# Kernel tuning notes

Measured on AMD Instinct MI355X. Metric: run time of the kernel, lower is better.

The kernel has to match this reference:

```python
import math
import jax, jax.numpy as jnp
import numpy as np

D = 256      # embedding_dim (= internal_dim, downsample_rate 1)
H = 8        # num_heads
HD = D // H  # head_dim = 32
NTC = 16     # num_text_classes
NIMG = 4096  # image tokens (64x64)
N = NIMG + NTC
B = 2
NKE = 64     # num_k_exclude_rope


def _rope(x, freqs):
    # x: (b, h, n, c); freqs: (n, c//2, 2) = (cos, sin) of complex rotary factors
    b, h, n, c = x.shape
    xp = x.reshape(b, h, n, c // 2, 2)
    cos, sin = freqs[..., 0], freqs[..., 1]
    xr, xi = xp[..., 0], xp[..., 1]
    out_r = xr * cos - xi * sin
    out_i = xr * sin + xi * cos
    return jnp.stack([out_r, out_i], axis=-1).reshape(b, h, n, c)


def _sep_heads(x):
    b, n, c = x.shape
    return x.reshape(b, n, H, c // H).transpose(0, 2, 1, 3)  # (b,h,n,hd)


def setup_inputs() -> dict:
    key = jax.random.key(0)
    ks = jax.random.split(key, 14)
    s = 0.02
    # rotary factors: unit-norm cos/sin pairs
    ang_img = jax.random.uniform(ks[3], (NIMG, HD // 2)) * (2.0 * np.pi)
    ang_txt = jax.random.uniform(ks[4], (NTC, HD // 2)) * (2.0 * np.pi)
    return {
        "q": jax.random.normal(ks[0], (B, N, D), dtype=jnp.float32),
        "k": jax.random.normal(ks[1], (B, N, D), dtype=jnp.float32),
        "v": jax.random.normal(ks[2], (B, N, D), dtype=jnp.float32),
        "freqs_cis_img": jnp.stack([jnp.cos(ang_img), jnp.sin(ang_img)], axis=-1),
        "freqs_cis_txt": jnp.stack([jnp.cos(ang_txt), jnp.sin(ang_txt)], axis=-1),
        "Wq": jax.random.normal(ks[5], (D, D), dtype=jnp.float32) * s,
        "bq": jnp.zeros((D,), dtype=jnp.float32),
        "Wk": jax.random.normal(ks[6], (D, D), dtype=jnp.float32) * s,
        "bk": jnp.zeros((D,), dtype=jnp.float32),
        "Wv": jax.random.normal(ks[7], (D, D), dtype=jnp.float32) * s,
        "bv": jnp.zeros((D,), dtype=jnp.float32),
        "Wo": jax.random.normal(ks[8], (D, D), dtype=jnp.float32) * s,
        "bo": jnp.zeros((D,), dtype=jnp.float32),
        "num_k_exclude_rope": NKE,
    }


def reference(q, k, v, freqs_cis_img, freqs_cis_txt,
              Wq, bq, Wk, bk, Wv, bv, Wo, bo, num_k_exclude_rope):
    q = q @ Wq.T + bq
    k = k @ Wk.T + bk
    v = v @ Wv.T + bv
    q = _sep_heads(q)  # (b,h,n,hd)
    k = _sep_heads(k)
    v = _sep_heads(v)

    # split tokens into image / text regions, apply RoPE separately
    q_img, q_txt = q[:, :, :-NTC, :], q[:, :, -NTC:, :]
    k_img, k_txt = k[:, :, :-NTC, :], k[:, :, -NTC:, :]
    q_img = _rope(q_img, freqs_cis_img)
    k_img = _rope(k_img, freqs_cis_img)
    q_txt = _rope(q_txt, freqs_cis_txt)
    k_txt = _rope(k_txt, freqs_cis_txt)
    q = jnp.concatenate([q_img, q_txt], axis=-2)
    k = jnp.concatenate([k_img, k_txt], axis=-2)

    scale = 1.0 / math.sqrt(HD)
    nke = num_k_exclude_rope
    if nke > 0:
        k_td, k_mem = k[:, :, :-nke, :], k[:, :, -nke:, :]
        v_td, v_mem = v[:, :, :-nke, :], v[:, :, -nke:, :]
        attn = jax.nn.softmax(jnp.einsum('bhqd,bhkd->bhqk', q, k_td) * scale, axis=-1)
        out = jnp.einsum('bhqk,bhkd->bhqd', attn, v_td)
        attn_m = jax.nn.softmax(jnp.einsum('bhqd,bhkd->bhqk', q, k_mem) * scale, axis=-1)
        out = out + jnp.einsum('bhqk,bhkd->bhqd', attn_m, v_mem)
    else:
        attn = jax.nn.softmax(jnp.einsum('bhqd,bhkd->bhqk', q, k) * scale, axis=-1)
        out = jnp.einsum('bhqk,bhkd->bhqd', attn, v)

    b, h, n, hd = out.shape
    out = out.transpose(0, 2, 1, 3).reshape(b, n, h * hd)
    return out @ Wo.T + bo
```

## Files before the change

kernel.cpp:

```cpp
#include <hip/hip_runtime.h>
#include <hip/hip_bf16.h>

#define BN    4112
#define NKR   4160
#define BNP   4160
#define BB    2
#define HH    8
#define NIMG_ 4096
#define NMAIN 4048
#define MROWS 8224
#define QSCALE 0.25505402f

typedef __attribute__((ext_vector_type(8))) short short8;
typedef __attribute__((ext_vector_type(4))) float f32x4;

__device__ __forceinline__ unsigned short f2bs(float x) { return __bfloat16_as_ushort(__float2bfloat16(x)); }
__device__ __forceinline__ unsigned pkbf(float a, float b) {
    __hip_bfloat162 h = __float22bfloat162_rn(make_float2(a, b));
    unsigned u; __builtin_memcpy(&u, &h, 4); return u;
}
__device__ __forceinline__ float fexp2(float x) {
#if __has_builtin(__builtin_amdgcn_exp2f)
    return __builtin_amdgcn_exp2f(x);
#else
    return exp2f(x);
#endif
}

__global__ __launch_bounds__(256)
void qkv_mfma(const float* __restrict__ Aq, const float* __restrict__ Ak, const float* __restrict__ Av,
              const float* __restrict__ Wq, const float* __restrict__ Wk, const float* __restrict__ Wv,
              const float* __restrict__ bq, const float* __restrict__ bk, const float* __restrict__ bv,
              short* __restrict__ Qr, short* __restrict__ Kr, short* __restrict__ Vt,
              const float* __restrict__ fimg, const float* __restrict__ ftxt)
{
    __shared__ __align__(16) short Ws[2][64][72];
    __shared__ __align__(16) short Ds[2][64][72];

    const int mode = blockIdx.z;
    const float* A    = (mode == 0) ? Aq : (mode == 1) ? Ak : Av;
    const float* W    = (mode == 0) ? Wq : (mode == 1) ? Wk : Wv;
    const float* bias = (mode == 0) ? bq : (mode == 1) ? bk : bv;

    const int t    = threadIdx.x;
    const int wave = t >> 6, lane = t & 63, q16 = lane & 15, quad = lane >> 4;
    const int f0 = blockIdx.x * 64;
    const int m0 = blockIdx.y * 64;
    const int sr = t >> 2, sc = (t & 3) * 16;
    const int arow = m0 + sr;
    const bool aval = arow < MROWS;
    const float* wp = W + (size_t)(f0 + sr) * 256 + sc;
    const float* ap = A + (size_t)(aval ? arow : 0) * 256 + sc;

    f32x4 acc[4] = {{0,0,0,0},{0,0,0,0},{0,0,0,0},{0,0,0,0}};

    uint4 wr0, wr1, dr0, dr1;
    {
        float4 a0 = *(const float4*)(wp),     a1 = *(const float4*)(wp + 4);
        float4 a2 = *(const float4*)(wp + 8), a3 = *(const float4*)(wp + 12);
        wr0 = uint4{pkbf(a0.x,a0.y), pkbf(a0.z,a0.w), pkbf(a1.x,a1.y), pkbf(a1.z,a1.w)};
        wr1 = uint4{pkbf(a2.x,a2.y), pkbf(a2.z,a2.w), pkbf(a3.x,a3.y), pkbf(a3.z,a3.w)};
        a0 = *(const float4*)(ap);     a1 = *(const float4*)(ap + 4);
        a2 = *(const float4*)(ap + 8); a3 = *(const float4*)(ap + 12);
        dr0 = uint4{pkbf(a0.x,a0.y), pkbf(a0.z,a0.w), pkbf(a1.x,a1.y), pkbf(a1.z,a1.w)};
        dr1 = uint4{pkbf(a2.x,a2.y), pkbf(a2.z,a2.w), pkbf(a3.x,a3.y), pkbf(a3.z,a3.w)};
    }
    *(uint4*)&Ws[0][sr][sc] = wr0; *(uint4*)&Ws[0][sr][sc + 8] = wr1;
    *(uint4*)&Ds[0][sr][sc] = dr0; *(uint4*)&Ds[0][sr][sc + 8] = dr1;
    __syncthreads();

    #pragma unroll
    for (int ki = 0; ki < 4; ++ki) {
        const int buf = ki & 1;
        if (ki < 3) {
            const int k1 = (ki + 1) * 64;
            float4 a0 = *(const float4*)(wp + k1),     a1 = *(const float4*)(wp + k1 + 4);
            float4 a2 = *(const float4*)(wp + k1 + 8), a3 = *(const float4*)(wp + k1 + 12);
            wr0 = uint4{pkbf(a0.x,a0.y), pkbf(a0.z,a0.w), pkbf(a1.x,a1.y), pkbf(a1.z,a1.w)};
            wr1 = uint4{pkbf(a2.x,a2.y), pkbf(a2.z,a2.w), pkbf(a3.x,a3.y), pkbf(a3.z,a3.w)};
            a0 = *(const float4*)(ap + k1);     a1 = *(const float4*)(ap + k1 + 4);
            a2 = *(const float4*)(ap + k1 + 8); a3 = *(const float4*)(ap + k1 + 12);
            dr0 = uint4{pkbf(a0.x,a0.y), pkbf(a0.z,a0.w), pkbf(a1.x,a1.y), pkbf(a1.z,a1.w)};
            dr1 = uint4{pkbf(a2.x,a2.y), pkbf(a2.z,a2.w), pkbf(a3.x,a3.y), pkbf(a3.z,a3.w)};
        }
        #pragma unroll
        for (int ks = 0; ks < 2; ++ks) {
            const short8 af = *(const short8*)&Ws[buf][wave * 16 + q16][ks * 32 + quad * 8];
            #pragma unroll
            for (int ct = 0; ct < 4; ++ct) {
                const short8 bf = *(const short8*)&Ds[buf][ct * 16 + q16][ks * 32 + quad * 8];
                acc[ct] = __builtin_amdgcn_mfma_f32_16x16x32_bf16(af, bf, acc[ct], 0, 0, 0);
            }
        }
        if (ki < 3) {
            *(uint4*)&Ws[buf ^ 1][sr][sc] = wr0; *(uint4*)&Ws[buf ^ 1][sr][sc + 8] = wr1;
            *(uint4*)&Ds[buf ^ 1][sr][sc] = dr0; *(uint4*)&Ds[buf ^ 1][sr][sc + 8] = dr1;
            __syncthreads();
        }
    }

    const int fbase = f0 + wave * 16 + quad * 4;
    const float4 bb = *(const float4*)(bias + fbase);
    float vs[4][4];
    #pragma unroll
    for (int ct = 0; ct < 4; ++ct) {
        int n = m0 + ct * 16 + q16;
        float v0 = acc[ct][0] + bb.x, v1 = acc[ct][1] + bb.y;
        float v2 = acc[ct][2] + bb.z, v3 = acc[ct][3] + bb.w;
        int b  = (n >= BN) ? 1 : 0;
        int nb = n - b * BN;
        if (mode < 2) {
            int j0 = (fbase & 31) >> 1;
            const float* fr = (nb < NIMG_) ? (fimg + ((size_t)nb * 16 + j0) * 2)
                                           : (ftxt + ((size_t)(nb - NIMG_) * 16 + j0) * 2);
            float4 cs = *(const float4*)fr;
            float r0 = v0 * cs.x - v1 * cs.y, i0 = v0 * cs.y + v1 * cs.x;
            float r1 = v2 * cs.z - v3 * cs.w, i1 = v2 * cs.w + v3 * cs.z;
            v0 = r0; v1 = i0; v2 = r1; v3 = i1;
        }
        if (mode == 2) {
            vs[ct][0] = v0; vs[ct][1] = v1; vs[ct][2] = v2; vs[ct][3] = v3;
            continue;
        }
        if (n >= MROWS) continue;
        const int h = (fbase >> 5) & 7, hd = fbase & 31;
        if (mode == 0) {
            unsigned short* op = (unsigned short*)Qr + (((size_t)(b * HH + h) * BN + nb) * 32 + hd);
            *(uint2*)op = uint2{pkbf(v0 * QSCALE, v1 * QSCALE), pkbf(v2 * QSCALE, v3 * QSCALE)};
        } else {
            int nk = nb + ((nb >= NMAIN) ? 48 : 0);
            unsigned short* op = (unsigned short*)Kr + (((size_t)(b * HH + h) * NKR + nk) * 32 + hd);
            *(uint2*)op = uint2{pkbf(v0, v1), pkbf(v2, v3)};
        }
    }

    if (mode == 2) {
        short (*Tr)[72] = Ds[0];
        const int fl = wave * 16 + quad * 4;
        #pragma unroll
        for (int ct = 0; ct < 4; ++ct) {
            const int nl = ct * 16 + q16;
            Tr[fl + 0][nl] = (short)f2bs(vs[ct][0]);
            Tr[fl + 1][nl] = (short)f2bs(vs[ct][1]);
            Tr[fl + 2][nl] = (short)f2bs(vs[ct][2]);
            Tr[fl + 3][nl] = (short)f2bs(vs[ct][3]);
        }
        __syncthreads();
        const int h0 = (f0 >> 5) & 7;
        #pragma unroll
        for (int ii = 0; ii < 2; ++ii) {
            const int r  = ii * 32 + (t >> 3);
            const int c8 = (t & 7) * 8;
            const int ng = m0 + c8;
            if (ng < MROWS) {
                uint4 val = *(const uint4*)&Tr[r][c8];
                int b  = (ng >= BN) ? 1 : 0;
                int nb = ng - b * BN;
                int nk = nb + ((nb >= NMAIN) ? 48 : 0);
                int h  = h0 + (r >> 5), hd = r & 31;
                unsigned short* op = (unsigned short*)Vt + ((size_t)(b * HH + h) * 32 + hd) * BNP + nk;
                *(uint4*)op = val;
            }
        }
    }

    if (blockIdx.x == 0 && blockIdx.y < 16 && t < 192) {
        const int bh = blockIdx.y;
        if (mode == 1) {
            short* base = Kr + (size_t)bh * NKR * 32 + (size_t)NMAIN * 32;
            *(uint4*)(base + t * 8) = uint4{0u, 0u, 0u, 0u};
        } else if (mode == 2) {
            short* base = Vt + (size_t)bh * 32 * BNP + (size_t)(t / 6) * BNP + NMAIN + (t % 6) * 8;
            *(uint4*)base = uint4{0u, 0u, 0u, 0u};
        }
    }
}

__global__ __launch_bounds__(256)
void attn_mfma(const short* __restrict__ Qr, const short* __restrict__ Kr,
               const short* __restrict__ Vt, unsigned short* __restrict__ AO)
{
    __shared__ __align__(16) short Ks[3][64][40];
    __shared__ __align__(16) short Vs[3][32][72];
    __shared__ __align__(16) short Ps[2][4][16][72];

    const int t    = threadIdx.x;
    const int wave = t >> 6, lane = t & 63, q16 = lane & 15, quad = lane >> 4;
    const int bh = blockIdx.y;
    const int q  = blockIdx.x * 64 + wave * 16 + q16;
    const int qc = (q < BN) ? q : (BN - 1);
    const short8 qf = *(const short8*)(Qr + ((size_t)bh * BN + qc) * 32 + quad * 8);

    f32x4 oA0 = {0,0,0,0}, oA1 = {0,0,0,0}, oB0 = {0,0,0,0}, oB1 = {0,0,0,0};
    float LA = 0.f, LB = 0.f;

    const int kr = t >> 2, kc = t & 3;
    const int vr = t >> 3, vc = t & 7;
    const short* kg = Kr + (size_t)bh * NKR * 32 + (size_t)kr * 32 + kc * 8;
    const short* vg = Vt + (size_t)bh * 32 * BNP + (size_t)vr * BNP + vc * 8;

    auto qk = [&](int buf, int pb) -> float {
        float lsum = 0.f;
        #pragma unroll
        for (int mt = 0; mt < 4; ++mt) {
            const short8 kf = *(const short8*)&Ks[buf][mt * 16 + q16][quad * 8];
            f32x4 z = {0,0,0,0};
            f32x4 s = __builtin_amdgcn_mfma_f32_16x16x32_bf16(kf, qf, z, 0, 0, 0);
            float p0 = fexp2(s[0]), p1 = fexp2(s[1]), p2 = fexp2(s[2]), p3 = fexp2(s[3]);
            lsum += (p0 + p1) + (p2 + p3);
            *(uint2*)&Ps[pb][wave][q16][mt * 16 + quad * 4] = uint2{pkbf(p0, p1), pkbf(p2, p3)};
        }
        return lsum;
    };
    auto pv = [&](int buf, int pb, f32x4& o0, f32x4& o1) {
        const short8 p0  = *(const short8*)&Ps[pb][wave][q16][quad * 8];
        const short8 p1  = *(const short8*)&Ps[pb][wave][q16][32 + quad * 8];
        const short8 v00 = *(const short8*)&Vs[buf][q16][quad * 8];
        const short8 v01 = *(const short8*)&Vs[buf][q16][32 + quad * 8];
        const short8 v10 = *(const short8*)&Vs[buf][16 + q16][quad * 8];
        const short8 v11 = *(const short8*)&Vs[buf][16 + q16][32 + quad * 8];
        o0 = __builtin_amdgcn_mfma_f32_16x16x32_bf16(v00, p0, o0, 0, 0, 0);
        o0 = __builtin_amdgcn_mfma_f32_16x16x32_bf16(v01, p1, o0, 0, 0, 0);
        o1 = __builtin_amdgcn_mfma_f32_16x16x32_bf16(v10, p0, o1, 0, 0, 0);
        o1 = __builtin_amdgcn_mfma_f32_16x16x32_bf16(v11, p1, o1, 0, 0, 0);
    };

    uint4 kA = *(const uint4*)(kg),        vA = *(const uint4*)(vg);
    *(uint4*)&Ks[0][kr][kc * 8] = kA;  *(uint4*)&Vs[0][vr][vc * 8] = vA;
    __syncthreads();
    kA = *(const uint4*)(kg + 2048);   vA = *(const uint4*)(vg + 64);
    LA += qk(0, 0);
    *(uint4*)&Ks[1][kr][kc * 8] = kA;  *(uint4*)&Vs[1][vr][vc * 8] = vA;
    __syncthreads();
    kA = *(const uint4*)(kg + 2 * 2048); vA = *(const uint4*)(vg + 2 * 64);

    int bc = 0, bn = 1, bp = 2, pc = 0;
    for (int it = 0; it < 64; ++it) {
        uint4 kN, vN;
        const bool pre = (it + 3) <= 64;
        if (pre) { kN = *(const uint4*)(kg + (size_t)(it + 3) * 2048);
                   vN = *(const uint4*)(vg + (it + 3) * 64); }
        float ls = qk(bn, pc ^ 1);
        if (it < 63) LA += ls; else LB += ls;
        pv(bc, pc, oA0, oA1);
        if (it + 2 <= 64) { *(uint4*)&Ks[bp][kr][kc * 8] = kA;
                            *(uint4*)&Vs[bp][vr][vc * 8] = vA; }
        if (pre) { kA = kN; vA = vN; }
        __syncthreads();
        int tmp = bc; bc = bn; bn = bp; bp = tmp; pc ^= 1;
    }
    pv(bc, pc, oB0, oB1);

    LA += __shfl_xor(LA, 16); LA += __shfl_xor(LA, 32);
    LB += __shfl_xor(LB, 16); LB += __shfl_xor(LB, 32);
    LA -= 48.f;

    if (q < BN) {
        const float iA = 1.f / LA, iB = 1.f / LB;
        const int b = bh >> 3, h = bh & 7;
        unsigned short* ap = AO + ((size_t)b * BN + q) * 256 + h * 32;
        float w0[4], w1[4];
        #pragma unroll
        for (int r = 0; r < 4; ++r) {
            w0[r] = oA0[r] * iA + oB0[r] * iB;
            w1[r] = oA1[r] * iA + oB1[r] * iB;
        }
        *(uint2*)(ap + quad * 4)      = uint2{pkbf(w0[0], w0[1]), pkbf(w0[2], w0[3])};
        *(uint2*)(ap + 16 + quad * 4) = uint2{pkbf(w1[0], w1[1]), pkbf(w1[2], w1[3])};
    }
}

__global__ __launch_bounds__(256)
void gemm_out(const unsigned short* __restrict__ A, const float* __restrict__ W,
              const float* __restrict__ bias, float* __restrict__ out)
{
    __shared__ __align__(16) short Ws[2][64][72];
    __shared__ __align__(16) short Ds[2][64][72];
    const int t    = threadIdx.x;
    const int wave = t >> 6, lane = t & 63, q16 = lane & 15, quad = lane >> 4;
    const int f0 = blockIdx.x * 64, m0 = blockIdx.y * 64;
    const int sr = t >> 2, sc = (t & 3) * 16;
    const int arow = m0 + sr;
    const bool aval = arow < MROWS;
    const float* wp = W + (size_t)(f0 + sr) * 256 + sc;
    const unsigned short* ap = A + (size_t)(aval ? arow : 0) * 256 + sc;

    f32x4 acc[4] = {{0,0,0,0},{0,0,0,0},{0,0,0,0},{0,0,0,0}};

    uint4 wr0, wr1, dr0, dr1;
    {
        float4 a0 = *(const float4*)(wp),     a1 = *(const float4*)(wp + 4);
        float4 a2 = *(const float4*)(wp + 8), a3 = *(const float4*)(wp + 12);
        wr0 = uint4{pkbf(a0.x,a0.y), pkbf(a0.z,a0.w), pkbf(a1.x,a1.y), pkbf(a1.z,a1.w)};
        wr1 = uint4{pkbf(a2.x,a2.y), pkbf(a2.z,a2.w), pkbf(a3.x,a3.y), pkbf(a3.z,a3.w)};
        dr0 = *(const uint4*)(ap); dr1 = *(const uint4*)(ap + 8);
    }
    *(uint4*)&Ws[0][sr][sc] = wr0; *(uint4*)&Ws[0][sr][sc + 8] = wr1;
    *(uint4*)&Ds[0][sr][sc] = dr0; *(uint4*)&Ds[0][sr][sc + 8] = dr1;
    __syncthreads();

    #pragma unroll
    for (int ki = 0; ki < 4; ++ki) {
        const int buf = ki & 1;
        if (ki < 3) {
            const int k1 = (ki + 1) * 64;
            float4 a0 = *(const float4*)(wp + k1),     a1 = *(const float4*)(wp + k1 + 4);
            float4 a2 = *(const float4*)(wp + k1 + 8), a3 = *(const float4*)(wp + k1 + 12);
            wr0 = uint4{pkbf(a0.x,a0.y), pkbf(a0.z,a0.w), pkbf(a1.x,a1.y), pkbf(a1.z,a1.w)};
            wr1 = uint4{pkbf(a2.x,a2.y), pkbf(a2.z,a2.w), pkbf(a3.x,a3.y), pkbf(a3.z,a3.w)};
            dr0 = *(const uint4*)(ap + k1); dr1 = *(const uint4*)(ap + k1 + 8);
        }
        #pragma unroll
        for (int ks = 0; ks < 2; ++ks) {
            const short8 af = *(const short8*)&Ws[buf][wave * 16 + q16][ks * 32 + quad * 8];
            #pragma unroll
            for (int ct = 0; ct < 4; ++ct) {
                const short8 bf = *(const short8*)&Ds[buf][ct * 16 + q16][ks * 32 + quad * 8];
                acc[ct] = __builtin_amdgcn_mfma_f32_16x16x32_bf16(af, bf, acc[ct], 0, 0, 0);
            }
        }
        if (ki < 3) {
            *(uint4*)&Ws[buf ^ 1][sr][sc] = wr0; *(uint4*)&Ws[buf ^ 1][sr][sc + 8] = wr1;
            *(uint4*)&Ds[buf ^ 1][sr][sc] = dr0; *(uint4*)&Ds[buf ^ 1][sr][sc + 8] = dr1;
            __syncthreads();
        }
    }

    const int fbase = f0 + wave * 16 + quad * 4;
    const float4 bb = *(const float4*)(bias + fbase);
    #pragma unroll
    for (int ct = 0; ct < 4; ++ct) {
        int n = m0 + ct * 16 + q16;
        if (n >= MROWS) continue;
        float* op = out + (size_t)n * 256 + fbase;
        *(float4*)op = float4{acc[ct][0] + bb.x, acc[ct][1] + bb.y,
                              acc[ct][2] + bb.z, acc[ct][3] + bb.w};
    }
}

extern "C" void kernel_launch(void* const* d_in, const int* in_sizes, int n_in,
                              void* d_out, int out_size, void* d_ws, size_t ws_size,
                              hipStream_t stream)
{
    (void)in_sizes; (void)n_in; (void)out_size; (void)ws_size;
    const float* q    = (const float*)d_in[0];
    const float* k    = (const float*)d_in[1];
    const float* v    = (const float*)d_in[2];
    const float* fimg = (const float*)d_in[3];
    const float* ftxt = (const float*)d_in[4];
    const float* Wq   = (const float*)d_in[5];
    const float* bq   = (const float*)d_in[6];
    const float* Wk   = (const float*)d_in[7];
    const float* bk   = (const float*)d_in[8];
    const float* Wv   = (const float*)d_in[9];
    const float* bv   = (const float*)d_in[10];
    const float* Wo   = (const float*)d_in[11];
    const float* bo   = (const float*)d_in[12];

    char* w = (char*)d_ws;
    short*          Qr = (short*)(w);
    short*          Kr = (short*)(w + 4210688);
    short*          Vt = (short*)(w + 8470528);
    unsigned short* AO = (unsigned short*)(w + 12730368);

    qkv_mfma<<<dim3(4, 129, 3), 256, 0, stream>>>(q, k, v, Wq, Wk, Wv, bq, bk, bv,
                                                  Qr, Kr, Vt, fimg, ftxt);
    attn_mfma<<<dim3(65, 16), 256, 0, stream>>>(Qr, Kr, Vt, AO);
    gemm_out<<<dim3(4, 129), 256, 0, stream>>>(AO, Wo, bo, (float*)d_out);
}
```

Measured before the change: 234.4 us.

## Keep softmax probabilities in registers and double-buffer K/V tiles

The attention loop no longer stages P through shared memory. Each pair of QK MFMA outputs is exponentiated, packed to bf16 and fed directly as the B operand of the PV MFMA, with the V fragments gathered to match that register layout. The three-stage K/V ring plus P double buffer becomes a simple two-stage ring, which cuts LDS traffic and footprint. The cost is less software pipelining overlap between QK and PV, plus more scattered 32-bit LDS reads for V.

```diff
diff --git a/kernel.cpp b/kernel.cpp
--- a/kernel.cpp
+++ b/kernel.cpp
@@ -180,9 +180,8 @@
 void attn_mfma(const short* __restrict__ Qr, const short* __restrict__ Kr,
                const short* __restrict__ Vt, unsigned short* __restrict__ AO)
 {
-    __shared__ __align__(16) short Ks[3][64][40];
-    __shared__ __align__(16) short Vs[3][32][72];
-    __shared__ __align__(16) short Ps[2][4][16][72];
+    __shared__ __align__(16) short Ks[2][64][40];
+    __shared__ __align__(16) short Vs[2][32][72];
 
     const int t    = threadIdx.x;
     const int wave = t >> 6, lane = t & 63, q16 = lane & 15, quad = lane >> 4;
@@ -199,57 +198,52 @@
     const short* kg = Kr + (size_t)bh * NKR * 32 + (size_t)kr * 32 + kc * 8;
     const short* vg = Vt + (size_t)bh * 32 * BNP + (size_t)vr * BNP + vc * 8;
 
-    auto qk = [&](int buf, int pb) -> float {
+    auto tile = [&](int buf, f32x4& o0, f32x4& o1, float& L) {
         float lsum = 0.f;
         #pragma unroll
-        for (int mt = 0; mt < 4; ++mt) {
-            const short8 kf = *(const short8*)&Ks[buf][mt * 16 + q16][quad * 8];
+        for (int g = 0; g < 2; ++g) {
+            const short8 kf0 = *(const short8*)&Ks[buf][(2*g)     * 16 + q16][quad * 8];
+            const short8 kf1 = *(const short8*)&Ks[buf][(2*g + 1) * 16 + q16][quad * 8];
             f32x4 z = {0,0,0,0};
-            f32x4 s = __builtin_amdgcn_mfma_f32_16x16x32_bf16(kf, qf, z, 0, 0, 0);
-            float p0 = fexp2(s[0]), p1 = fexp2(s[1]), p2 = fexp2(s[2]), p3 = fexp2(s[3]);
-            lsum += (p0 + p1) + (p2 + p3);
-            *(uint2*)&Ps[pb][wave][q16][mt * 16 + quad * 4] = uint2{pkbf(p0, p1), pkbf(p2, p3)};
-        }
-        return lsum;
+            f32x4 s0 = __builtin_amdgcn_mfma_f32_16x16x32_bf16(kf0, qf, z, 0, 0, 0);
+            f32x4 s1 = __builtin_amdgcn_mfma_f32_16x16x32_bf16(kf1, qf, z, 0, 0, 0);
+            float p0 = fexp2(s0[0]), p1 = fexp2(s0[1]), p2 = fexp2(s0[2]), p3 = fexp2(s0[3]);
+            float p4 = fexp2(s1[0]), p5 = fexp2(s1[1]), p6 = fexp2(s1[2]), p7 = fexp2(s1[3]);
+            lsum += ((p0 + p1) + (p2 + p3)) + ((p4 + p5) + (p6 + p7));
+            uint4 pbu = uint4{pkbf(p0, p1), pkbf(p2, p3), pkbf(p4, p5), pkbf(p6, p7)};
+            short8 pb; __builtin_memcpy(&pb, &pbu, 16);
+            uint2 va0 = uint2{*(const unsigned*)&Vs[buf][q16][g*32 + quad*4],
+                              *(const unsigned*)&Vs[buf][q16][g*32 + quad*4 + 2]};
+            uint2 va1 = uint2{*(const unsigned*)&Vs[buf][q16][g*32 + 16 + quad*4],
+                              *(const unsigned*)&Vs[buf][q16][g*32 + 16 + quad*4 + 2]};
+            uint4 vau = uint4{va0.x, va0.y, va1.x, va1.y};
+            short8 vf; __builtin_memcpy(&vf, &vau, 16);
+            o0 = __builtin_amdgcn_mfma_f32_16x16x32_bf16(vf, pb, o0, 0, 0, 0);
+            uint2 vb0 = uint2{*(const unsigned*)&Vs[buf][16 + q16][g*32 + quad*4],
+                              *(const unsigned*)&Vs[buf][16 + q16][g*32 + quad*4 + 2]};
+            uint2 vb1 = uint2{*(const unsigned*)&Vs[buf][16 + q16][g*32 + 16 + quad*4],
+                              *(const unsigned*)&Vs[buf][16 + q16][g*32 + 16 + quad*4 + 2]};
+            uint4 vbu = uint4{vb0.x, vb0.y, vb1.x, vb1.y};
+            short8 vg2; __builtin_memcpy(&vg2, &vbu, 16);
+            o1 = __builtin_amdgcn_mfma_f32_16x16x32_bf16(vg2, pb, o1, 0, 0, 0);
+        }
+        L += lsum;
     };
-    auto pv = [&](int buf, int pb, f32x4& o0, f32x4& o1) {
-        const short8 p0  = *(const short8*)&Ps[pb][wave][q16][quad * 8];
-        const short8 p1  = *(const short8*)&Ps[pb][wave][q16][32 + quad * 8];
-        const short8 v00 = *(const short8*)&Vs[buf][q16][quad * 8];
-        const short8 v01 = *(const short8*)&Vs[buf][q16][32 + quad * 8];
-        const short8 v10 = *(const short8*)&Vs[buf][16 + q16][quad * 8];
-        const short8 v11 = *(const short8*)&Vs[buf][16 + q16][32 + quad * 8];
-        o0 = __builtin_amdgcn_mfma_f32_16x16x32_bf16(v00, p0, o0, 0, 0, 0);
-        o0 = __builtin_amdgcn_mfma_f32_16x16x32_bf16(v01, p1, o0, 0, 0, 0);
-        o1 = __builtin_amdgcn_mfma_f32_16x16x32_bf16(v10, p0, o1, 0, 0, 0);
-        o1 = __builtin_amdgcn_mfma_f32_16x16x32_bf16(v11, p1, o1, 0, 0, 0);
-    };
-
-    uint4 kA = *(const uint4*)(kg),        vA = *(const uint4*)(vg);
-    *(uint4*)&Ks[0][kr][kc * 8] = kA;  *(uint4*)&Vs[0][vr][vc * 8] = vA;
+
+    *(uint4*)&Ks[0][kr][kc * 8] = *(const uint4*)(kg);
+    *(uint4*)&Vs[0][vr][vc * 8] = *(const uint4*)(vg);
     __syncthreads();
-    kA = *(const uint4*)(kg + 2048);   vA = *(const uint4*)(vg + 64);
-    LA += qk(0, 0);
-    *(uint4*)&Ks[1][kr][kc * 8] = kA;  *(uint4*)&Vs[1][vr][vc * 8] = vA;
-    __syncthreads();
-    kA = *(const uint4*)(kg + 2 * 2048); vA = *(const uint4*)(vg + 2 * 64);
-
-    int bc = 0, bn = 1, bp = 2, pc = 0;
+
     for (int it = 0; it < 64; ++it) {
-        uint4 kN, vN;
-        const bool pre = (it + 3) <= 64;
-        if (pre) { kN = *(const uint4*)(kg + (size_t)(it + 3) * 2048);
-                   vN = *(const uint4*)(vg + (it + 3) * 64); }
-        float ls = qk(bn, pc ^ 1);
-        if (it < 63) LA += ls; else LB += ls;
-        pv(bc, pc, oA0, oA1);
-        if (it + 2 <= 64) { *(uint4*)&Ks[bp][kr][kc * 8] = kA;
-                            *(uint4*)&Vs[bp][vr][vc * 8] = vA; }
-        if (pre) { kA = kN; vA = vN; }
+        const int buf = it & 1;
+        uint4 kreg = *(const uint4*)(kg + (size_t)(it + 1) * 2048);
+        uint4 vreg = *(const uint4*)(vg + (it + 1) * 64);
+        tile(buf, oA0, oA1, LA);
+        *(uint4*)&Ks[buf ^ 1][kr][kc * 8] = kreg;
+        *(uint4*)&Vs[buf ^ 1][vr][vc * 8] = vreg;
         __syncthreads();
-        int tmp = bc; bc = bn; bn = bp; bp = tmp; pc ^= 1;
-    }
-    pv(bc, pc, oB0, oB1);
+    }
+    tile(0, oB0, oB1, LB);
 
     LA += __shfl_xor(LA, 16); LA += __shfl_xor(LA, 32);
     LB += __shfl_xor(LB, 16); LB += __shfl_xor(LB, 32);
```

Result: faster. 207.5 us (-11.5%).
